# Performance work log

Measured on AMD Instinct MI355X. Metric: run time of the kernel, lower is better.

## Reference

```python
import jax, jax.numpy as jnp
import numpy as np

B, N, D, T = 64, 512, 128, 8  # batch, atoms, atom_embedding_dim, num_bond_types
NEG_SLOPE = 0.2


def setup_inputs() -> dict:
    key = jax.random.key(0)
    k1, k2, k3, k4 = jax.random.split(key, 4)
    src = jax.random.normal(k1, (B, N, D), dtype=jnp.float32)
    dst = jax.random.normal(k2, (B, N, D), dtype=jnp.float32)
    # bond-type index per (i,j) pair; -1 means 'no bond' (masked)
    edges = jax.random.randint(k3, (B, N, N), -1, T, dtype=jnp.int32)
    # xavier_uniform with gain=1.414 on shape (2*D*T, 1)
    fan_in, fan_out = 2 * D * T, 1
    bound = 1.414 * np.sqrt(6.0 / (fan_in + fan_out))
    a = jax.random.uniform(k4, (2 * D * T, 1), minval=-bound, maxval=bound,
                           dtype=jnp.float32)
    return {"src_embeddings": src, "dst_embeddings": dst, "edges": edges, "a": a}


def reference(src_embeddings, dst_embeddings, edges, a):
    b, n, d = src_embeddings.shape
    t = a.shape[0] // (2 * d)
    # a row-block k (length 2d) is the weight for bond type k:
    # score = a_k[:d] . src_i + a_k[d:] . dst_j
    a_mat = a.reshape(t, 2 * d)
    a_src, a_dst = a_mat[:, :d], a_mat[:, d:]
    s_src = jnp.einsum('bnd,td->bnt', src_embeddings, a_src)  # (B,N,T)
    s_dst = jnp.einsum('bnd,td->bnt', dst_embeddings, a_dst)  # (B,N,T)
    k = jnp.clip(edges, 0, t - 1)                             # (B,N,N)
    bi = jnp.arange(b)[:, None, None]
    gi = jnp.arange(n)[None, :, None]
    gj = jnp.arange(n)[None, None, :]
    g = s_src[bi, gi, k] + s_dst[bi, gj, k]                   # (B,N,N)
    scores = jnp.where(edges >= 0, g, jnp.zeros((), g.dtype))
    return jnp.where(scores >= 0, scores, NEG_SLOPE * scores)
```

## Files before the change

### kernel.cpp

```cpp
#include <hip/hip_runtime.h>

#define BB 64
#define NN 512
#define DD 128
#define TT 8
#define NEG_SLOPE 0.2f

typedef float f32x4 __attribute__((ext_vector_type(4)));
typedef int i32x4 __attribute__((ext_vector_type(4)));

__global__ __launch_bounds__(256) void precompute_scores(
    const float* __restrict__ src, const float* __restrict__ dst,
    const float* __restrict__ a, float* __restrict__ s_src,
    float* __restrict__ s_dstT) {
  const int tid = threadIdx.x;
  const int wave = tid >> 6, lane = tid & 63;
  const int t = lane & 7, dc = lane >> 3;
  const int d0 = dc * 16;
  const int r0 = (blockIdx.x * 4 + wave) * 8;

  f32x4 as[4], ad[4];
#pragma unroll
  for (int i = 0; i < 4; ++i) {
    as[i] = *(const f32x4*)(a + t * 2 * DD + d0 + 4 * i);
    ad[i] = *(const f32x4*)(a + t * 2 * DD + DD + d0 + 4 * i);
  }

  float ps[8], pd[8];
#pragma unroll
  for (int ri = 0; ri < 8; ++ri) {
    const long r = r0 + ri;
    float p = 0.f, q = 0.f;
#pragma unroll
    for (int i = 0; i < 4; ++i) {
      const f32x4 x = *(const f32x4*)(src + r * DD + d0 + 4 * i);
      p += x.x * as[i].x + x.y * as[i].y + x.z * as[i].z + x.w * as[i].w;
      const f32x4 y = *(const f32x4*)(dst + r * DD + d0 + 4 * i);
      q += y.x * ad[i].x + y.y * ad[i].y + y.z * ad[i].z + y.w * ad[i].w;
    }
    p += __shfl_xor(p, 8, 64);
    p += __shfl_xor(p, 16, 64);
    p += __shfl_xor(p, 32, 64);
    q += __shfl_xor(q, 8, 64);
    q += __shfl_xor(q, 16, 64);
    q += __shfl_xor(q, 32, 64);
    ps[ri] = p;
    pd[ri] = q;
  }

  float vs = ps[0], vd = pd[0];
#pragma unroll
  for (int ri = 1; ri < 8; ++ri) {
    vs = dc == ri ? ps[ri] : vs;
    vd = dc == ri ? pd[ri] : vd;
  }
  const int rr = r0 + dc;
  s_src[(long)rr * TT + t] = vs;
  const int b = rr >> 9, n = rr & 511;
  s_dstT[((long)b * TT + t) * NN + n] = vd;
}

__global__ __launch_bounds__(512) void edge_attention(
    const int* __restrict__ edges, const float* __restrict__ s_src,
    const float* __restrict__ s_dstT, float* __restrict__ out) {
  __shared__ float sdt[NN * 9];
  __shared__ float ssc[32 * TT];

  const int tid = threadIdx.x;
  const int b = blockIdx.x >> 4;
  const int i0 = (blockIdx.x & 15) * 32;

  const float* __restrict__ g_sdt = s_dstT + (long)b * NN * TT;
#pragma unroll
  for (int q = 0; q < TT; ++q) sdt[tid * 9 + q] = g_sdt[q * NN + tid];

  if (tid < 64) {
    ((f32x4*)ssc)[tid] =
        ((const f32x4*)(s_src + ((long)b * NN + i0) * TT))[tid];
  }
  __syncthreads();

  const int rsub = tid >> 7;
  const int j0 = (tid & 127) * 4;

#pragma unroll 4
  for (int it = 0; it < 8; ++it) {
    const int r = it * 4 + rsub;
    const long base = ((long)(b * NN + i0 + r)) * NN + j0;
    const i32x4 e4 = *(const i32x4*)(edges + base);
    const float* __restrict__ sr = ssc + r * TT;

    const int ee[4] = {e4.x, e4.y, e4.z, e4.w};
    float oo[4];
#pragma unroll
    for (int m = 0; m < 4; ++m) {
      const int e = ee[m];
      const int k = e < 0 ? 0 : e;
      const float g = sr[k] + sdt[(j0 + m) * 9 + k];
      const float v = e < 0 ? 0.0f : g;
      oo[m] = v >= 0.0f ? v : NEG_SLOPE * v;
    }
    const f32x4 o = {oo[0], oo[1], oo[2], oo[3]};
    __builtin_nontemporal_store(o, (f32x4*)(out + base));
  }
}

extern "C" void kernel_launch(void* const* d_in, const int* in_sizes, int n_in,
                              void* d_out, int out_size, void* d_ws, size_t ws_size,
                              hipStream_t stream) {
  const float* src = (const float*)d_in[0];
  const float* dst = (const float*)d_in[1];
  const int* edges = (const int*)d_in[2];
  const float* a = (const float*)d_in[3];
  float* out = (float*)d_out;

  float* s_src = (float*)d_ws;
  float* s_dstT = s_src + (long)BB * NN * TT;

  precompute_scores<<<1024, 256, 0, stream>>>(src, dst, a, s_src, s_dstT);

  edge_attention<<<BB * 16, 512, 0, stream>>>(edges, s_src, s_dstT, out);
}
```

Before: 165.6 us.

## Hold dst scores in registers and select bond type with branchless muxes

```diff
diff --git a/kernel.cpp b/kernel.cpp
--- a/kernel.cpp
+++ b/kernel.cpp
@@ -60,48 +60,61 @@
   s_dstT[((long)b * TT + t) * NN + n] = vd;
 }
 
-__global__ __launch_bounds__(512) void edge_attention(
+__global__ __launch_bounds__(256) void edge_attention(
     const int* __restrict__ edges, const float* __restrict__ s_src,
     const float* __restrict__ s_dstT, float* __restrict__ out) {
-  __shared__ float sdt[NN * 9];
-  __shared__ float ssc[32 * TT];
+  __shared__ float ssc[16 * TT];
 
   const int tid = threadIdx.x;
-  const int b = blockIdx.x >> 4;
-  const int i0 = (blockIdx.x & 15) * 32;
+  const int wave = tid >> 6, lane = tid & 63;
+  const int bid = blockIdx.x;
+  const int jhalf = bid & 1;
+  const int itile = (bid >> 1) & 31;
+  const int b = bid >> 6;
+  const int i0 = itile * 16;
+  const int j0 = jhalf * 256 + lane * 4;
 
-  const float* __restrict__ g_sdt = s_dstT + (long)b * NN * TT;
+  const float* __restrict__ sdb = s_dstT + (long)b * NN * TT;
+  f32x4 sd[TT];
 #pragma unroll
-  for (int q = 0; q < TT; ++q) sdt[tid * 9 + q] = g_sdt[q * NN + tid];
+  for (int t = 0; t < TT; ++t) sd[t] = *(const f32x4*)(sdb + t * NN + j0);
 
-  if (tid < 64) {
+  i32x4 e4[4];
+#pragma unroll
+  for (int it = 0; it < 4; ++it) {
+    const long rbase = ((long)(b * NN + i0 + it * 4 + wave)) * NN + j0;
+    e4[it] = *(const i32x4*)(edges + rbase);
+  }
+
+  if (tid < 32) {
     ((f32x4*)ssc)[tid] =
         ((const f32x4*)(s_src + ((long)b * NN + i0) * TT))[tid];
   }
   __syncthreads();
 
-  const int rsub = tid >> 7;
-  const int j0 = (tid & 127) * 4;
-
-#pragma unroll 4
-  for (int it = 0; it < 8; ++it) {
-    const int r = it * 4 + rsub;
-    const long base = ((long)(b * NN + i0 + r)) * NN + j0;
-    const i32x4 e4 = *(const i32x4*)(edges + base);
-    const float* __restrict__ sr = ssc + r * TT;
-
-    const int ee[4] = {e4.x, e4.y, e4.z, e4.w};
+#pragma unroll
+  for (int it = 0; it < 4; ++it) {
+    const int r = it * 4 + wave;
+    const long rbase = ((long)(b * NN + i0 + r)) * NN + j0;
+    const int es[4] = {e4[it].x, e4[it].y, e4[it].z, e4[it].w};
     float oo[4];
 #pragma unroll
     for (int m = 0; m < 4; ++m) {
-      const int e = ee[m];
+      const int e = es[m];
       const int k = e < 0 ? 0 : e;
-      const float g = sr[k] + sdt[(j0 + m) * 9 + k];
-      const float v = e < 0 ? 0.0f : g;
-      oo[m] = v >= 0.0f ? v : NEG_SLOPE * v;
+      const float a0 = (k & 1) ? sd[1][m] : sd[0][m];
+      const float a1 = (k & 1) ? sd[3][m] : sd[2][m];
+      const float a2 = (k & 1) ? sd[5][m] : sd[4][m];
+      const float a3 = (k & 1) ? sd[7][m] : sd[6][m];
+      const float b0 = (k & 2) ? a1 : a0;
+      const float b1 = (k & 2) ? a3 : a2;
+      const float dsel = (k & 4) ? b1 : b0;
+      const float g = ssc[r * TT + k] + dsel;
+      const float w = fmaxf(g, NEG_SLOPE * g);
+      oo[m] = e < 0 ? 0.0f : w;
     }
     const f32x4 o = {oo[0], oo[1], oo[2], oo[3]};
-    __builtin_nontemporal_store(o, (f32x4*)(out + base));
+    *(f32x4*)(out + rbase) = o;
   }
 }
 
@@ -119,5 +132,5 @@
 
   precompute_scores<<<1024, 256, 0, stream>>>(src, dst, a, s_src, s_dstT);
 
-  edge_attention<<<BB * 16, 512, 0, stream>>>(edges, s_src, s_dstT, out);
+  edge_attention<<<BB * 64, 256, 0, stream>>>(edges, s_src, s_dstT, out);
 }
```

New measurement: 158.0 us. -4.6%, faster.
